# Kernel optimization log

Measured on AMD Instinct MI355X. Metric: run time of the kernel, lower is better.

## Reference

```python
import jax, jax.numpy as jnp
import numpy as np

N = 100000      # total nodes (flattened batch)
E = 640000      # total edges
D = 128         # in_channels
SIM_THR = 0.2   # pt_dict['sim_pt']
DEG_THR = 3.0   # pt_dict['degree_pt']
PT_THRESHOLD = 0.1  # edge-pruning cosine threshold
EPS = 1e-8      # F.cosine_similarity eps


def _glorot(key, shape):
    a = np.sqrt(6.0 / (shape[-2] + shape[-1]))
    return jax.random.uniform(key, shape, jnp.float32, -a, a)


def setup_inputs() -> dict:
    key = jax.random.key(0)
    k1, k2, k3, k4, k5 = jax.random.split(key, 5)
    x = jax.random.normal(k1, (N, D), jnp.float32)
    edge_index = jax.random.randint(k2, (2, E), 0, N, dtype=jnp.int32)
    p_sim = _glorot(k3, (1, D))
    p_deg = _glorot(k4, (1, D))
    p_other = _glorot(k5, (1, D))
    return {"x": x, "edge_index": edge_index, "p_sim": p_sim, "p_deg": p_deg, "p_other": p_other}


def reference(x, edge_index, p_sim, p_deg, p_other):
    n = x.shape[0]
    row, col = edge_index[0], edge_index[1]

    # --- sim_pt: per-edge cosine of raw features, scatter-add to dst, degree-normalize ---
    x_norm = x / jnp.sqrt(jnp.sum(x * x, axis=1, keepdims=True))          # [N, D]
    e = jnp.sum(x_norm[row] * x_norm[col], axis=1)                         # [E]
    c = jax.ops.segment_sum(e, col, num_segments=n)                        # [N]
    deg = jax.ops.segment_sum(jnp.ones_like(e), col, num_segments=n)       # [N]
    # torch: c/deg -> nan for deg==0, nan <= thr is False; +inf gives the same mask, safely.
    csim = jnp.where(deg > 0, c / jnp.maximum(deg, 1.0), jnp.inf)
    mask_sim = csim <= SIM_THR                                             # [N]

    # --- degree_pt ---
    mask_deg = deg <= DEG_THR                                              # [N]

    # --- other_pt == 'all': nodes that got no prompt so far ---
    mask_other = ~(mask_sim | mask_deg)                                    # [N]

    # g_mutiftpt_record: [N, 3, D], slot filled with its prompt row where mask else 0
    masks = jnp.stack([mask_sim, mask_deg, mask_other], axis=1)            # [N, 3]
    prompts = jnp.concatenate([p_sim, p_deg, p_other], axis=0)             # [3, D]
    record = masks[:, :, None].astype(x.dtype) * prompts[None, :, :]       # [N, 3, D]

    # use_attention=False branch: mean over non-padding (all-nonzero) slots
    wo_pad = jnp.all(record != 0, axis=-1)                                 # [N, 3]
    plen = jnp.sum(wo_pad, axis=1, keepdims=True).astype(x.dtype)          # [N, 1]
    final = jnp.where(plen > 0, record.sum(axis=1) / jnp.maximum(plen, 1.0), 0.0)  # [N, D]

    x_new = x + final                                                      # add_pt

    # edge pruning by cosine similarity of prompted features (F.cosine_similarity, eps=1e-8)
    nrm = jnp.sqrt(jnp.sum(x_new * x_new, axis=1))                         # [N]
    na = jnp.maximum(nrm[row], EPS)
    nb = jnp.maximum(nrm[col], EPS)
    cos = jnp.sum(x_new[row] * x_new[col], axis=1) / (na * nb)             # [E]
    keep_edges = cos >= PT_THRESHOLD                                       # [E] bool mask (edge list is static-shape; mask instead of compaction)
    return x_new, keep_edges
```

## Files before the change

### kernel.cpp

```cpp
#include <hip/hip_runtime.h>
#include <hip/hip_bf16.h>
#include <math.h>

#define D_DIM 128
#define SIM_THR 0.2f
#define DEG_THR 3.0f
#define PT_THR 0.1
#define EPS_CS 1e-8
#define MARGIN 4e-3f
#define PK 4294967296.0

typedef unsigned short u16;

#define WS_NEED 8960064

__device__ __forceinline__ float bf2f(u16 u) {
    return __uint_as_float(((unsigned)u) << 16);
}

__global__ void prompt_pre_kernel(const float* __restrict__ ps,
                                  const float* __restrict__ pd,
                                  const float* __restrict__ po,
                                  int* __restrict__ flags,
                                  float* __restrict__ G) {
    int t = threadIdx.x;
    float s0 = ps[t], s1 = ps[t + 64];
    float d0 = pd[t], d1 = pd[t + 64];
    float o0 = po[t], o1 = po[t + 64];
    float ss = s0 * s0 + s1 * s1;
    float sd = s0 * d0 + s1 * d1;
    float so = s0 * o0 + s1 * o1;
    float dd = d0 * d0 + d1 * d1;
    float dO = d0 * o0 + d1 * o1;
    float oo = o0 * o0 + o1 * o1;
    for (int m = 32; m; m >>= 1) {
        ss += __shfl_xor(ss, m);
        sd += __shfl_xor(sd, m);
        so += __shfl_xor(so, m);
        dd += __shfl_xor(dd, m);
        dO += __shfl_xor(dO, m);
        oo += __shfl_xor(oo, m);
    }
    unsigned long long zs = __ballot(s0 == 0.0f || s1 == 0.0f);
    unsigned long long zd = __ballot(d0 == 0.0f || d1 == 0.0f);
    unsigned long long zo = __ballot(o0 == 0.0f || o1 == 0.0f);
    if (t == 0) {
        flags[0] = (zs == 0ull);
        flags[1] = (zd == 0ull);
        flags[2] = (zo == 0ull);
        G[0] = ss; G[1] = sd; G[2] = so;
        G[3] = sd; G[4] = dd; G[5] = dO;
        G[6] = so; G[7] = dO; G[8] = oo;
    }
}

__global__ void node_pre_kernel(const float* __restrict__ x,
                                const float* __restrict__ ps,
                                const float* __restrict__ pd,
                                const float* __restrict__ po,
                                u16* __restrict__ xnorm,
                                float* __restrict__ nx,
                                float* __restrict__ rs,
                                float* __restrict__ rd,
                                float* __restrict__ ro, int N) {
    int g = threadIdx.x >> 5;
    int lane = threadIdx.x & 31;
    int n = blockIdx.x * 8 + g;
    if (n >= N) return;
    int off = lane * 4;
    const float4 v = *(const float4*)(x + (size_t)n * D_DIM + off);
    const float4 s = *(const float4*)(ps + off);
    const float4 d = *(const float4*)(pd + off);
    const float4 o = *(const float4*)(po + off);
    float sq = v.x * v.x + v.y * v.y + v.z * v.z + v.w * v.w;
    float drs = v.x * s.x + v.y * s.y + v.z * s.z + v.w * s.w;
    float drd = v.x * d.x + v.y * d.y + v.z * d.z + v.w * d.w;
    float dro = v.x * o.x + v.y * o.y + v.z * o.z + v.w * o.w;
    for (int m = 16; m; m >>= 1) {
        sq += __shfl_xor(sq, m, 32);
        drs += __shfl_xor(drs, m, 32);
        drd += __shfl_xor(drd, m, 32);
        dro += __shfl_xor(dro, m, 32);
    }
    float nrm = sqrtf(sq);
    float inv = 1.0f / nrm;
    __hip_bfloat16 ob[4];
    ob[0] = __float2bfloat16(v.x * inv);
    ob[1] = __float2bfloat16(v.y * inv);
    ob[2] = __float2bfloat16(v.z * inv);
    ob[3] = __float2bfloat16(v.w * inv);
    *(ushort4*)(xnorm + (size_t)n * D_DIM + off) =
        make_ushort4(*(u16*)&ob[0], *(u16*)&ob[1], *(u16*)&ob[2], *(u16*)&ob[3]);
    if (lane == 0) {
        nx[n] = nrm;
        rs[n] = drs;
        rd[n] = drd;
        ro[n] = dro;
    }
}

__global__ void edge_sim_kernel(const u16* __restrict__ xnorm,
                                const int* __restrict__ ei,
                                double* __restrict__ cd,
                                float* __restrict__ e_arr,
                                int E) {
    int lane = threadIdx.x & 31;
    int grp = blockIdx.x * 8 + (threadIdx.x >> 5);
    int base = grp * 4;
    if (base >= E) return;

    int r[4], c4[4];
    #pragma unroll
    for (int k = 0; k < 4; ++k) {
        int e = base + k;
        int src = (e < E) ? e : base;
        r[k] = ei[src];
        c4[k] = ei[E + src];
    }

    ushort4 a[4], b[4];
    #pragma unroll
    for (int k = 0; k < 4; ++k) {
        a[k] = *(const ushort4*)(xnorm + (size_t)r[k] * D_DIM + lane * 4);
        b[k] = *(const ushort4*)(xnorm + (size_t)c4[k] * D_DIM + lane * 4);
    }

    float d[4];
    #pragma unroll
    for (int k = 0; k < 4; ++k) {
        d[k] = bf2f(a[k].x) * bf2f(b[k].x) + bf2f(a[k].y) * bf2f(b[k].y) +
               bf2f(a[k].z) * bf2f(b[k].z) + bf2f(a[k].w) * bf2f(b[k].w);
    }
    for (int m = 16; m; m >>= 1) {
        #pragma unroll
        for (int k = 0; k < 4; ++k) d[k] += __shfl_xor(d[k], m, 32);
    }

    if (lane < 4) {
        int e = base + lane;
        if (e < E) {
            float dv = (lane == 0) ? d[0] : (lane == 1) ? d[1] : (lane == 2) ? d[2] : d[3];
            if (e_arr) e_arr[e] = dv;
            atomicAdd(&cd[c4[lane]], (double)dv + PK);
        }
    }
}

__global__ void node_prompt_kernel(const float* __restrict__ x,
                                   const double* __restrict__ cd,
                                   const float* __restrict__ ps,
                                   const float* __restrict__ pd,
                                   const float* __restrict__ po,
                                   const int* __restrict__ flags,
                                   const float* __restrict__ nx,
                                   const float* __restrict__ rs,
                                   const float* __restrict__ rd,
                                   const float* __restrict__ ro,
                                   float* __restrict__ xn,
                                   double* __restrict__ na,
                                   float* __restrict__ pack, int N) {
    int g = threadIdx.x >> 5;
    int lane = threadIdx.x & 31;
    int n = blockIdx.x * 8 + g;
    if (n >= N) return;
    double v = cd[n];
    double degd = floor(v * (1.0 / PK) + 0.5);
    float dg = (float)degd;
    float cc = (float)(v - degd * PK);
    float csim = (dg > 0.0f) ? (cc / fmaxf(dg, 1.0f)) : INFINITY;
    bool ms = (csim <= SIM_THR);
    bool md = (dg <= DEG_THR);
    bool mo = !(ms || md);
    int plen = (ms && flags[0]) + (md && flags[1]) + (mo && flags[2]);
    float invp = (plen > 0) ? (1.0f / (float)plen) : 0.0f;

    int off = lane * 4;
    const float4 xv = *(const float4*)(x + (size_t)n * D_DIM + off);
    const float4 s  = *(const float4*)(ps + off);
    const float4 dd = *(const float4*)(pd + off);
    const float4 o  = *(const float4*)(po + off);

    float4 f;
    f.x = (ms ? s.x : 0.0f) + (md ? dd.x : 0.0f) + (mo ? o.x : 0.0f);
    f.y = (ms ? s.y : 0.0f) + (md ? dd.y : 0.0f) + (mo ? o.y : 0.0f);
    f.z = (ms ? s.z : 0.0f) + (md ? dd.z : 0.0f) + (mo ? o.z : 0.0f);
    f.w = (ms ? s.w : 0.0f) + (md ? dd.w : 0.0f) + (mo ? o.w : 0.0f);

    float4 r;
    r.x = xv.x + f.x * invp;
    r.y = xv.y + f.y * invp;
    r.z = xv.z + f.z * invp;
    r.w = xv.w + f.w * invp;

    *(float4*)(xn + (size_t)n * D_DIM + off) = r;

    double sq = (double)r.x * r.x + (double)r.y * r.y + (double)r.z * r.z + (double)r.w * r.w;
    for (int m = 16; m; m >>= 1) sq += __shfl_xor(sq, m, 32);
    if (lane == 0) {
        double nrm = sqrt(sq);
        double nad = (nrm > EPS_CS) ? nrm : EPS_CS;
        na[n] = nad;
        if (pack) {
            float as = ms ? invp : 0.0f;
            float ad = md ? invp : 0.0f;
            float ao = mo ? invp : 0.0f;
            float4 w0 = make_float4(rs[n], rd[n], ro[n], nx[n]);
            float4 w1 = make_float4(as, ad, ao, (float)(1.0 / nad));
            *(float4*)(pack + (size_t)n * 8)     = w0;
            *(float4*)(pack + (size_t)n * 8 + 4) = w1;
        }
    }
}

__global__ void edge_prune_fused(const int* __restrict__ ei,
                                 const float* __restrict__ e_arr,
                                 const float* __restrict__ pack,
                                 const float* __restrict__ G,
                                 const float* __restrict__ xn,
                                 const double* __restrict__ na,
                                 float* __restrict__ keep, int E) {
    __shared__ int s_list[256];
    __shared__ int s_cnt;
    int tid = threadIdx.x;
    if (tid == 0) s_cnt = 0;
    __syncthreads();

    int e = blockIdx.x * 256 + tid;
    if (e < E) {
        int i = ei[e], j = ei[E + e];
        const float4 ri = *(const float4*)(pack + (size_t)i * 8);
        const float4 ai = *(const float4*)(pack + (size_t)i * 8 + 4);
        const float4 rj = *(const float4*)(pack + (size_t)j * 8);
        const float4 aj = *(const float4*)(pack + (size_t)j * 8 + 4);
        float ev = e_arr[e];
        float dot = ev * ri.w * rj.w
                  + aj.x * ri.x + aj.y * ri.y + aj.z * ri.z
                  + ai.x * rj.x + ai.y * rj.y + ai.z * rj.z;
        dot += ai.x * (G[0] * aj.x + G[1] * aj.y + G[2] * aj.z)
             + ai.y * (G[3] * aj.x + G[4] * aj.y + G[5] * aj.z)
             + ai.z * (G[6] * aj.x + G[7] * aj.y + G[8] * aj.z);
        float cosv = dot * ai.w * aj.w;
        keep[e] = (cosv >= 0.1f) ? 1.0f : 0.0f;
        if (fabsf(cosv - 0.1f) < MARGIN) {
            int idx = atomicAdd(&s_cnt, 1);
            s_list[idx] = e;
        }
    }
    __syncthreads();

    int cnt = s_cnt;
    int lane = tid & 31;
    int grp = tid >> 5;
    for (int it = grp; it < cnt; it += 8) {
        int ee = s_list[it];
        int row = ei[ee], col = ei[E + ee];
        const float4 a = *(const float4*)(xn + (size_t)row * D_DIM + lane * 4);
        const float4 b = *(const float4*)(xn + (size_t)col * D_DIM + lane * 4);
        double d = (double)a.x * b.x + (double)a.y * b.y +
                   (double)a.z * b.z + (double)a.w * b.w;
        for (int m = 16; m; m >>= 1) d += __shfl_xor(d, m, 32);
        if (lane == 0) {
            double cs = d / (na[row] * na[col]);
            keep[ee] = (cs >= PT_THR) ? 1.0f : 0.0f;
        }
    }
}

__global__ void edge_prune_kernel(const float* __restrict__ xn,
                                  const int* __restrict__ ei,
                                  const double* __restrict__ na,
                                  float* __restrict__ keep, int E) {
    int lane = threadIdx.x & 31;
    int grp = blockIdx.x * 8 + (threadIdx.x >> 5);
    int e0 = grp * 2, e1 = e0 + 1;
    if (e0 >= E) return;
    bool has1 = (e1 < E);
    int row0 = ei[e0], col0 = ei[E + e0];
    int row1 = has1 ? ei[e1] : row0;
    int col1 = has1 ? ei[E + e1] : col0;

    const float4 a0 = *(const float4*)(xn + (size_t)row0 * D_DIM + lane * 4);
    const float4 b0 = *(const float4*)(xn + (size_t)col0 * D_DIM + lane * 4);
    const float4 a1 = *(const float4*)(xn + (size_t)row1 * D_DIM + lane * 4);
    const float4 b1 = *(const float4*)(xn + (size_t)col1 * D_DIM + lane * 4);

    double d0 = (double)a0.x * b0.x + (double)a0.y * b0.y +
                (double)a0.z * b0.z + (double)a0.w * b0.w;
    double d1 = (double)a1.x * b1.x + (double)a1.y * b1.y +
                (double)a1.z * b1.z + (double)a1.w * b1.w;
    for (int m = 16; m; m >>= 1) {
        d0 += __shfl_xor(d0, m, 32);
        d1 += __shfl_xor(d1, m, 32);
    }
    if (lane == 0) {
        double cs = d0 / (na[row0] * na[col0]);
        keep[e0] = (cs >= PT_THR) ? 1.0f : 0.0f;
    } else if (lane == 1 && has1) {
        double cs = d1 / (na[row1] * na[col1]);
        keep[e1] = (cs >= PT_THR) ? 1.0f : 0.0f;
    }
}

extern "C" void kernel_launch(void* const* d_in, const int* in_sizes, int n_in,
                              void* d_out, int out_size, void* d_ws, size_t ws_size,
                              hipStream_t stream) {
    const float* x  = (const float*)d_in[0];
    const int*   ei = (const int*)d_in[1];
    const float* ps = (const float*)d_in[2];
    const float* pd = (const float*)d_in[3];
    const float* po = (const float*)d_in[4];

    const int N = in_sizes[0] / D_DIM;
    const int E = in_sizes[1] / 2;

    float* xn    = (float*)d_out;
    float* keep  = (float*)d_out + (size_t)N * D_DIM;
    u16*   xnorm = (u16*)d_out;

    char* ws = (char*)d_ws;
    const int nodeBlocks = (N + 7) / 8;
    const int simBlocks  = (E + 31) / 32;

    if (ws_size >= (size_t)WS_NEED) {
        double* cd    = (double*)(ws + 0);
        double* na    = (double*)(ws + 800000);
        float* nx     = (float*)(ws + 1600000);
        float* rs     = (float*)(ws + 2000000);
        float* rd     = (float*)(ws + 2400000);
        float* ro     = (float*)(ws + 2800000);
        float* e_arr  = (float*)(ws + 3200000);
        float* pack   = (float*)(ws + 5760000);
        int*   flags  = (int*)(ws + 8960000);
        float* G      = (float*)(ws + 8960016);

        hipMemsetAsync(cd, 0, 800000, stream);

        prompt_pre_kernel<<<1, 64, 0, stream>>>(ps, pd, po, flags, G);
        node_pre_kernel<<<nodeBlocks, 256, 0, stream>>>(x, ps, pd, po, xnorm, nx, rs, rd, ro, N);
        edge_sim_kernel<<<simBlocks, 256, 0, stream>>>(xnorm, ei, cd, e_arr, E);
        node_prompt_kernel<<<nodeBlocks, 256, 0, stream>>>(x, cd, ps, pd, po,
                                                           flags, nx, rs, rd, ro,
                                                           xn, na, pack, N);
        edge_prune_fused<<<(E + 255) / 256, 256, 0, stream>>>(ei, e_arr, pack, G, xn, na, keep, E);
    } else {
        double* cd    = (double*)(ws + 0);
        double* na    = (double*)(ws + 800000);
        int*   flags  = (int*)(ws + 1600000);
        float* G      = (float*)(ws + 1600016);
        float* scratch = (float*)(ws + 1600064);

        hipMemsetAsync(cd, 0, 800000, stream);
        prompt_pre_kernel<<<1, 64, 0, stream>>>(ps, pd, po, flags, G);
        node_pre_kernel<<<nodeBlocks, 256, 0, stream>>>(x, ps, pd, po, xnorm,
                                                        scratch, scratch, scratch, scratch, N);
        edge_sim_kernel<<<simBlocks, 256, 0, stream>>>(xnorm, ei, cd, nullptr, E);
        node_prompt_kernel<<<nodeBlocks, 256, 0, stream>>>(x, cd, ps, pd, po,
                                                           flags, nullptr, nullptr, nullptr, nullptr,
                                                           xn, na, nullptr, N);
        edge_prune_kernel<<<(E + 15) / 16, 256, 0, stream>>>(xn, ei, na, keep, E);
    }
}
```

Before: 107.6 us.

## Quantize normalized features to fp8 with exact fixup for near-threshold nodes

Normalized node features are stored as packed fp8 e4m3 instead of bf16, which halves the gather traffic in the edge similarity pass. Per-edge similarities are saved as bf16. Nodes whose mean similarity falls within a margin of the threshold are marked in a bitmap, then recomputed exactly by a scan over all edges and a node fixup kernel. The memset and the prompt-precompute launch are folded into the first node kernel, and the prune-candidate list is bounded with an inline exact fallback when it overflows. In exchange this adds two extra launches, including a full edge scan, and relies on a fixed margin being wide enough to cover the fp8 error.

Result: slower. 115.6 us (+7.4%).

```diff
diff --git a/kernel.cpp b/kernel.cpp
--- a/kernel.cpp
+++ b/kernel.cpp
@@ -1,5 +1,6 @@
 #include <hip/hip_runtime.h>
 #include <hip/hip_bf16.h>
+#include <hip/hip_fp8.h>
 #include <math.h>
 
 #define D_DIM 128
@@ -7,103 +8,114 @@
 #define DEG_THR 3.0f
 #define PT_THR 0.1
 #define EPS_CS 1e-8
-#define MARGIN 4e-3f
+#define NODE_MARGIN 0.022f
+#define PRUNE_MARGIN 0.022f
 #define PK 4294967296.0
 
 typedef unsigned short u16;
-
-#define WS_NEED 8960064
+typedef unsigned int u32;
+
+#define WS_NEED 8092900
 
 __device__ __forceinline__ float bf2f(u16 u) {
-    return __uint_as_float(((unsigned)u) << 16);
-}
-
-__global__ void prompt_pre_kernel(const float* __restrict__ ps,
-                                  const float* __restrict__ pd,
-                                  const float* __restrict__ po,
-                                  int* __restrict__ flags,
-                                  float* __restrict__ G) {
-    int t = threadIdx.x;
-    float s0 = ps[t], s1 = ps[t + 64];
-    float d0 = pd[t], d1 = pd[t + 64];
-    float o0 = po[t], o1 = po[t + 64];
-    float ss = s0 * s0 + s1 * s1;
-    float sd = s0 * d0 + s1 * d1;
-    float so = s0 * o0 + s1 * o1;
-    float dd = d0 * d0 + d1 * d1;
-    float dO = d0 * o0 + d1 * o1;
-    float oo = o0 * o0 + o1 * o1;
-    for (int m = 32; m; m >>= 1) {
-        ss += __shfl_xor(ss, m);
-        sd += __shfl_xor(sd, m);
-        so += __shfl_xor(so, m);
-        dd += __shfl_xor(dd, m);
-        dO += __shfl_xor(dO, m);
-        oo += __shfl_xor(oo, m);
-    }
-    unsigned long long zs = __ballot(s0 == 0.0f || s1 == 0.0f);
-    unsigned long long zd = __ballot(d0 == 0.0f || d1 == 0.0f);
-    unsigned long long zo = __ballot(o0 == 0.0f || o1 == 0.0f);
-    if (t == 0) {
-        flags[0] = (zs == 0ull);
-        flags[1] = (zd == 0ull);
-        flags[2] = (zo == 0ull);
-        G[0] = ss; G[1] = sd; G[2] = so;
-        G[3] = sd; G[4] = dd; G[5] = dO;
-        G[6] = so; G[7] = dO; G[8] = oo;
-    }
-}
-
-__global__ void node_pre_kernel(const float* __restrict__ x,
-                                const float* __restrict__ ps,
-                                const float* __restrict__ pd,
-                                const float* __restrict__ po,
-                                u16* __restrict__ xnorm,
-                                float* __restrict__ nx,
-                                float* __restrict__ rs,
-                                float* __restrict__ rd,
-                                float* __restrict__ ro, int N) {
+    return __uint_as_float(((u32)u) << 16);
+}
+__device__ __forceinline__ float f8f(u32 v) {
+    __hip_fp8_e4m3 t;
+    t.__x = (__hip_fp8_storage_t)v;
+    return (float)t;
+}
+__device__ __forceinline__ u16 f2bf(float f) {
+    __hip_bfloat16 b = __float2bfloat16(f);
+    return *(u16*)&b;
+}
+
+__global__ void node_pre_fp8(const float* __restrict__ x,
+                             const float* __restrict__ ps,
+                             const float* __restrict__ pd,
+                             const float* __restrict__ po,
+                             u32* __restrict__ x8d,
+                             float* __restrict__ nx,
+                             float* __restrict__ rs,
+                             float* __restrict__ rd,
+                             float* __restrict__ ro,
+                             double* __restrict__ cd,
+                             u32* __restrict__ bitmap, int nbmw,
+                             int* __restrict__ flags,
+                             float* __restrict__ G, int N) {
     int g = threadIdx.x >> 5;
     int lane = threadIdx.x & 31;
     int n = blockIdx.x * 8 + g;
-    if (n >= N) return;
-    int off = lane * 4;
-    const float4 v = *(const float4*)(x + (size_t)n * D_DIM + off);
-    const float4 s = *(const float4*)(ps + off);
-    const float4 d = *(const float4*)(pd + off);
-    const float4 o = *(const float4*)(po + off);
-    float sq = v.x * v.x + v.y * v.y + v.z * v.z + v.w * v.w;
-    float drs = v.x * s.x + v.y * s.y + v.z * s.z + v.w * s.w;
-    float drd = v.x * d.x + v.y * d.y + v.z * d.z + v.w * d.w;
-    float dro = v.x * o.x + v.y * o.y + v.z * o.z + v.w * o.w;
-    for (int m = 16; m; m >>= 1) {
-        sq += __shfl_xor(sq, m, 32);
-        drs += __shfl_xor(drs, m, 32);
-        drd += __shfl_xor(drd, m, 32);
-        dro += __shfl_xor(dro, m, 32);
-    }
-    float nrm = sqrtf(sq);
-    float inv = 1.0f / nrm;
-    __hip_bfloat16 ob[4];
-    ob[0] = __float2bfloat16(v.x * inv);
-    ob[1] = __float2bfloat16(v.y * inv);
-    ob[2] = __float2bfloat16(v.z * inv);
-    ob[3] = __float2bfloat16(v.w * inv);
-    *(ushort4*)(xnorm + (size_t)n * D_DIM + off) =
-        make_ushort4(*(u16*)&ob[0], *(u16*)&ob[1], *(u16*)&ob[2], *(u16*)&ob[3]);
-    if (lane == 0) {
-        nx[n] = nrm;
-        rs[n] = drs;
-        rd[n] = drd;
-        ro[n] = dro;
-    }
-}
-
-__global__ void edge_sim_kernel(const u16* __restrict__ xnorm,
-                                const int* __restrict__ ei,
-                                double* __restrict__ cd,
-                                float* __restrict__ e_arr,
-                                int E) {
+    int gid = blockIdx.x * 256 + threadIdx.x;
+    if (gid < nbmw) bitmap[gid] = 0u;
+    if (n < N) {
+        int off = lane * 4;
+        const float4 v = *(const float4*)(x + (size_t)n * D_DIM + off);
+        const float4 s = *(const float4*)(ps + off);
+        const float4 d = *(const float4*)(pd + off);
+        const float4 o = *(const float4*)(po + off);
+        float sq = v.x * v.x + v.y * v.y + v.z * v.z + v.w * v.w;
+        float drs = v.x * s.x + v.y * s.y + v.z * s.z + v.w * s.w;
+        float drd = v.x * d.x + v.y * d.y + v.z * d.z + v.w * d.w;
+        float dro = v.x * o.x + v.y * o.y + v.z * o.z + v.w * o.w;
+        for (int m = 16; m; m >>= 1) {
+            sq += __shfl_xor(sq, m, 32);
+            drs += __shfl_xor(drs, m, 32);
+            drd += __shfl_xor(drd, m, 32);
+            dro += __shfl_xor(dro, m, 32);
+        }
+        float nrm = sqrtf(sq);
+        float inv = 1.0f / nrm;
+        __hip_fp8_e4m3 q0(v.x * inv), q1(v.y * inv), q2(v.z * inv), q3(v.w * inv);
+        u32 packed = (u32)q0.__x | ((u32)q1.__x << 8) |
+                     ((u32)q2.__x << 16) | ((u32)q3.__x << 24);
+        x8d[(size_t)n * 32 + lane] = packed;
+        if (lane == 0) {
+            nx[n] = nrm;
+            rs[n] = drs;
+            rd[n] = drd;
+            ro[n] = dro;
+            cd[n] = 0.0;
+        }
+    }
+    if (blockIdx.x == 0 && threadIdx.x < 64) {
+        int t = threadIdx.x;
+        float s0 = ps[t], s1 = ps[t + 64];
+        float d0 = pd[t], d1 = pd[t + 64];
+        float o0 = po[t], o1 = po[t + 64];
+        float ss = s0 * s0 + s1 * s1;
+        float sd = s0 * d0 + s1 * d1;
+        float so = s0 * o0 + s1 * o1;
+        float dd = d0 * d0 + d1 * d1;
+        float dO = d0 * o0 + d1 * o1;
+        float oo = o0 * o0 + o1 * o1;
+        for (int m = 32; m; m >>= 1) {
+            ss += __shfl_xor(ss, m);
+            sd += __shfl_xor(sd, m);
+            so += __shfl_xor(so, m);
+            dd += __shfl_xor(dd, m);
+            dO += __shfl_xor(dO, m);
+            oo += __shfl_xor(oo, m);
+        }
+        unsigned long long zs = __ballot(s0 == 0.0f || s1 == 0.0f);
+        unsigned long long zd = __ballot(d0 == 0.0f || d1 == 0.0f);
+        unsigned long long zo = __ballot(o0 == 0.0f || o1 == 0.0f);
+        if (t == 0) {
+            flags[0] = (zs == 0ull);
+            flags[1] = (zd == 0ull);
+            flags[2] = (zo == 0ull);
+            G[0] = ss; G[1] = sd; G[2] = so;
+            G[3] = sd; G[4] = dd; G[5] = dO;
+            G[6] = so; G[7] = dO; G[8] = oo;
+        }
+    }
+}
+
+__global__ void edge_sim_fp8(const u32* __restrict__ x8d,
+                             const int* __restrict__ ei,
+                             double* __restrict__ cd,
+                             u16* __restrict__ e_arr,
+                             int E) {
     int lane = threadIdx.x & 31;
     int grp = blockIdx.x * 8 + (threadIdx.x >> 5);
     int base = grp * 4;
@@ -117,30 +129,30 @@
         r[k] = ei[src];
         c4[k] = ei[E + src];
     }
-
-    ushort4 a[4], b[4];
+    u32 a[4], b[4];
     #pragma unroll
     for (int k = 0; k < 4; ++k) {
-        a[k] = *(const ushort4*)(xnorm + (size_t)r[k] * D_DIM + lane * 4);
-        b[k] = *(const ushort4*)(xnorm + (size_t)c4[k] * D_DIM + lane * 4);
-    }
-
+        a[k] = x8d[(size_t)r[k] * 32 + lane];
+        b[k] = x8d[(size_t)c4[k] * 32 + lane];
+    }
     float d[4];
     #pragma unroll
     for (int k = 0; k < 4; ++k) {
-        d[k] = bf2f(a[k].x) * bf2f(b[k].x) + bf2f(a[k].y) * bf2f(b[k].y) +
-               bf2f(a[k].z) * bf2f(b[k].z) + bf2f(a[k].w) * bf2f(b[k].w);
+        d[k] = f8f(a[k] & 255u) * f8f(b[k] & 255u) +
+               f8f((a[k] >> 8) & 255u) * f8f((b[k] >> 8) & 255u) +
+               f8f((a[k] >> 16) & 255u) * f8f((b[k] >> 16) & 255u) +
+               f8f(a[k] >> 24) * f8f(b[k] >> 24);
     }
     for (int m = 16; m; m >>= 1) {
         #pragma unroll
         for (int k = 0; k < 4; ++k) d[k] += __shfl_xor(d[k], m, 32);
     }
-
     if (lane < 4) {
         int e = base + lane;
         if (e < E) {
-            float dv = (lane == 0) ? d[0] : (lane == 1) ? d[1] : (lane == 2) ? d[2] : d[3];
-            if (e_arr) e_arr[e] = dv;
+            float dv = (lane == 0) ? d[0] : (lane == 1) ? d[1]
+                     : (lane == 2) ? d[2] : d[3];
+            e_arr[e] = f2bf(dv);
             atomicAdd(&cd[c4[lane]], (double)dv + PK);
         }
     }
@@ -158,7 +170,9 @@
                                    const float* __restrict__ ro,
                                    float* __restrict__ xn,
                                    double* __restrict__ na,
-                                   float* __restrict__ pack, int N) {
+                                   float* __restrict__ pack,
+                                   u32* __restrict__ bitmap,
+                                   float* __restrict__ cfix, int N) {
     int g = threadIdx.x >> 5;
     int lane = threadIdx.x & 31;
     int n = blockIdx.x * 8 + g;
@@ -200,20 +214,107 @@
         double nrm = sqrt(sq);
         double nad = (nrm > EPS_CS) ? nrm : EPS_CS;
         na[n] = nad;
-        if (pack) {
-            float as = ms ? invp : 0.0f;
-            float ad = md ? invp : 0.0f;
-            float ao = mo ? invp : 0.0f;
-            float4 w0 = make_float4(rs[n], rd[n], ro[n], nx[n]);
-            float4 w1 = make_float4(as, ad, ao, (float)(1.0 / nad));
-            *(float4*)(pack + (size_t)n * 8)     = w0;
-            *(float4*)(pack + (size_t)n * 8 + 4) = w1;
-        }
+        float as = ms ? invp : 0.0f;
+        float ad = md ? invp : 0.0f;
+        float ao = mo ? invp : 0.0f;
+        *(float4*)(pack + (size_t)n * 8)     = make_float4(rs[n], rd[n], ro[n], nx[n]);
+        *(float4*)(pack + (size_t)n * 8 + 4) = make_float4(as, ad, ao, (float)(1.0 / nad));
+        if (dg > 0.0f && fabsf(csim - SIM_THR) < NODE_MARGIN) {
+            cfix[n] = 0.0f;
+            atomicOr(&bitmap[n >> 5], 1u << (n & 31));
+        }
+    }
+}
+
+__global__ void edge_fix_scan(const float* __restrict__ x,
+                              const int* __restrict__ ei,
+                              const float* __restrict__ nx,
+                              const u32* __restrict__ bitmap,
+                              float* __restrict__ cfix, int E) {
+    int e = blockIdx.x * 256 + threadIdx.x;
+    if (e >= E) return;
+    int col = ei[E + e];
+    if (!((bitmap[col >> 5] >> (col & 31)) & 1u)) return;
+    int row = ei[e];
+    const float4* xr = (const float4*)(x + (size_t)row * D_DIM);
+    const float4* xc = (const float4*)(x + (size_t)col * D_DIM);
+    double s = 0.0;
+    for (int i = 0; i < 32; ++i) {
+        float4 a = xr[i], b = xc[i];
+        s += (double)a.x * b.x + (double)a.y * b.y +
+             (double)a.z * b.z + (double)a.w * b.w;
+    }
+    float ev = (float)(s / ((double)nx[row] * (double)nx[col]));
+    atomicAdd(&cfix[col], ev);
+}
+
+__global__ void node_fix_kernel(const float* __restrict__ x,
+                                const double* __restrict__ cd,
+                                const float* __restrict__ cfix,
+                                const u32* __restrict__ bitmap,
+                                const float* __restrict__ ps,
+                                const float* __restrict__ pd,
+                                const float* __restrict__ po,
+                                const int* __restrict__ flags,
+                                const float* __restrict__ nx,
+                                const float* __restrict__ rs,
+                                const float* __restrict__ rd,
+                                const float* __restrict__ ro,
+                                float* __restrict__ xn,
+                                double* __restrict__ na,
+                                float* __restrict__ pack, int N) {
+    int g = threadIdx.x >> 5;
+    int lane = threadIdx.x & 31;
+    int n = blockIdx.x * 8 + g;
+    if (n >= N) return;
+    if (!((bitmap[n >> 5] >> (n & 31)) & 1u)) return;
+
+    double v = cd[n];
+    double degd = floor(v * (1.0 / PK) + 0.5);
+    float dg = (float)degd;
+    float csim = cfix[n] / fmaxf(dg, 1.0f);
+    bool ms = (csim <= SIM_THR);
+    bool md = (dg <= DEG_THR);
+    bool mo = !(ms || md);
+    int plen = (ms && flags[0]) + (md && flags[1]) + (mo && flags[2]);
+    float invp = (plen > 0) ? (1.0f / (float)plen) : 0.0f;
+
+    int off = lane * 4;
+    const float4 xv = *(const float4*)(x + (size_t)n * D_DIM + off);
+    const float4 s  = *(const float4*)(ps + off);
+    const float4 dd = *(const float4*)(pd + off);
+    const float4 o  = *(const float4*)(po + off);
+
+    float4 f;
+    f.x = (ms ? s.x : 0.0f) + (md ? dd.x : 0.0f) + (mo ? o.x : 0.0f);
+    f.y = (ms ? s.y : 0.0f) + (md ? dd.y : 0.0f) + (mo ? o.y : 0.0f);
+    f.z = (ms ? s.z : 0.0f) + (md ? dd.z : 0.0f) + (mo ? o.z : 0.0f);
+    f.w = (ms ? s.w : 0.0f) + (md ? dd.w : 0.0f) + (mo ? o.w : 0.0f);
+
+    float4 r;
+    r.x = xv.x + f.x * invp;
+    r.y = xv.y + f.y * invp;
+    r.z = xv.z + f.z * invp;
+    r.w = xv.w + f.w * invp;
+
+    *(float4*)(xn + (size_t)n * D_DIM + off) = r;
+
+    double sq = (double)r.x * r.x + (double)r.y * r.y + (double)r.z * r.z + (double)r.w * r.w;
+    for (int m = 16; m; m >>= 1) sq += __shfl_xor(sq, m, 32);
+    if (lane == 0) {
+        double nrm = sqrt(sq);
+        double nad = (nrm > EPS_CS) ? nrm : EPS_CS;
+        na[n] = nad;
+        float as = ms ? invp : 0.0f;
+        float ad = md ? invp : 0.0f;
+        float ao = mo ? invp : 0.0f;
+        *(float4*)(pack + (size_t)n * 8)     = make_float4(rs[n], rd[n], ro[n], nx[n]);
+        *(float4*)(pack + (size_t)n * 8 + 4) = make_float4(as, ad, ao, (float)(1.0 / nad));
     }
 }
 
 __global__ void edge_prune_fused(const int* __restrict__ ei,
-                                 const float* __restrict__ e_arr,
+                                 const u16* __restrict__ e_arr,
                                  const float* __restrict__ pack,
                                  const float* __restrict__ G,
                                  const float* __restrict__ xn,
@@ -232,7 +333,7 @@
         const float4 ai = *(const float4*)(pack + (size_t)i * 8 + 4);
         const float4 rj = *(const float4*)(pack + (size_t)j * 8);
         const float4 aj = *(const float4*)(pack + (size_t)j * 8 + 4);
-        float ev = e_arr[e];
+        float ev = bf2f(e_arr[e]);
         float dot = ev * ri.w * rj.w
                   + aj.x * ri.x + aj.y * ri.y + aj.z * ri.z
                   + ai.x * rj.x + ai.y * rj.y + ai.z * rj.z;
@@ -241,14 +342,27 @@
              + ai.z * (G[6] * aj.x + G[7] * aj.y + G[8] * aj.z);
         float cosv = dot * ai.w * aj.w;
         keep[e] = (cosv >= 0.1f) ? 1.0f : 0.0f;
-        if (fabsf(cosv - 0.1f) < MARGIN) {
+        if (fabsf(cosv - 0.1f) < PRUNE_MARGIN) {
             int idx = atomicAdd(&s_cnt, 1);
-            s_list[idx] = e;
+            if (idx < 256) {
+                s_list[idx] = e;
+            } else {
+                const float4* xr = (const float4*)(xn + (size_t)i * D_DIM);
+                const float4* xc = (const float4*)(xn + (size_t)j * D_DIM);
+                double sd = 0.0;
+                for (int it = 0; it < 32; ++it) {
+                    float4 a = xr[it], b = xc[it];
+                    sd += (double)a.x * b.x + (double)a.y * b.y +
+                          (double)a.z * b.z + (double)a.w * b.w;
+                }
+                double cs = sd / (na[i] * na[j]);
+                keep[e] = (cs >= PT_THR) ? 1.0f : 0.0f;
+            }
         }
     }
     __syncthreads();
 
-    int cnt = s_cnt;
+    int cnt = s_cnt < 256 ? s_cnt : 256;
     int lane = tid & 31;
     int grp = tid >> 5;
     for (int it = grp; it < cnt; it += 8) {
@@ -266,10 +380,121 @@
     }
 }
 
-__global__ void edge_prune_kernel(const float* __restrict__ xn,
-                                  const int* __restrict__ ei,
-                                  const double* __restrict__ na,
-                                  float* __restrict__ keep, int E) {
+__global__ void node_pre_bf16(const float* __restrict__ x,
+                              const float* __restrict__ ps,
+                              const float* __restrict__ pd,
+                              const float* __restrict__ po,
+                              u16* __restrict__ xnorm,
+                              double* __restrict__ cd,
+                              int* __restrict__ flags, int N) {
+    int g = threadIdx.x >> 5;
+    int lane = threadIdx.x & 31;
+    int n = blockIdx.x * 8 + g;
+    if (n < N) {
+        int off = lane * 4;
+        const float4 v = *(const float4*)(x + (size_t)n * D_DIM + off);
+        float sq = v.x * v.x + v.y * v.y + v.z * v.z + v.w * v.w;
+        for (int m = 16; m; m >>= 1) sq += __shfl_xor(sq, m, 32);
+        float inv = 1.0f / sqrtf(sq);
+        *(ushort4*)(xnorm + (size_t)n * D_DIM + off) =
+            make_ushort4(f2bf(v.x * inv), f2bf(v.y * inv), f2bf(v.z * inv), f2bf(v.w * inv));
+        if (lane == 0) cd[n] = 0.0;
+    }
+    if (blockIdx.x == 0 && threadIdx.x < 64) {
+        int t = threadIdx.x;
+        unsigned long long zs = __ballot(ps[t] == 0.0f || ps[t + 64] == 0.0f);
+        unsigned long long zd = __ballot(pd[t] == 0.0f || pd[t + 64] == 0.0f);
+        unsigned long long zo = __ballot(po[t] == 0.0f || po[t + 64] == 0.0f);
+        if (t == 0) {
+            flags[0] = (zs == 0ull);
+            flags[1] = (zd == 0ull);
+            flags[2] = (zo == 0ull);
+        }
+    }
+}
+
+__global__ void edge_sim_bf16(const u16* __restrict__ xnorm,
+                              const int* __restrict__ ei,
+                              double* __restrict__ cd, int E) {
+    int lane = threadIdx.x & 31;
+    int grp = blockIdx.x * 8 + (threadIdx.x >> 5);
+    int base = grp * 4;
+    if (base >= E) return;
+    int r[4], c4[4];
+    #pragma unroll
+    for (int k = 0; k < 4; ++k) {
+        int e = base + k;
+        int src = (e < E) ? e : base;
+        r[k] = ei[src];
+        c4[k] = ei[E + src];
+    }
+    float d[4];
+    #pragma unroll
+    for (int k = 0; k < 4; ++k) {
+        ushort4 a = *(const ushort4*)(xnorm + (size_t)r[k] * D_DIM + lane * 4);
+        ushort4 b = *(const ushort4*)(xnorm + (size_t)c4[k] * D_DIM + lane * 4);
+        d[k] = bf2f(a.x) * bf2f(b.x) + bf2f(a.y) * bf2f(b.y) +
+               bf2f(a.z) * bf2f(b.z) + bf2f(a.w) * bf2f(b.w);
+    }
+    for (int m = 16; m; m >>= 1) {
+        #pragma unroll
+        for (int k = 0; k < 4; ++k) d[k] += __shfl_xor(d[k], m, 32);
+    }
+    if (lane < 4) {
+        int e = base + lane;
+        if (e < E) {
+            float dv = (lane == 0) ? d[0] : (lane == 1) ? d[1]
+                     : (lane == 2) ? d[2] : d[3];
+            atomicAdd(&cd[c4[lane]], (double)dv + PK);
+        }
+    }
+}
+
+__global__ void node_prompt_fb(const float* __restrict__ x,
+                               const double* __restrict__ cd,
+                               const float* __restrict__ ps,
+                               const float* __restrict__ pd,
+                               const float* __restrict__ po,
+                               const int* __restrict__ flags,
+                               float* __restrict__ xn,
+                               double* __restrict__ na, int N) {
+    int g = threadIdx.x >> 5;
+    int lane = threadIdx.x & 31;
+    int n = blockIdx.x * 8 + g;
+    if (n >= N) return;
+    double v = cd[n];
+    double degd = floor(v * (1.0 / PK) + 0.5);
+    float dg = (float)degd;
+    float cc = (float)(v - degd * PK);
+    float csim = (dg > 0.0f) ? (cc / fmaxf(dg, 1.0f)) : INFINITY;
+    bool ms = (csim <= SIM_THR);
+    bool md = (dg <= DEG_THR);
+    bool mo = !(ms || md);
+    int plen = (ms && flags[0]) + (md && flags[1]) + (mo && flags[2]);
+    float invp = (plen > 0) ? (1.0f / (float)plen) : 0.0f;
+    int off = lane * 4;
+    const float4 xv = *(const float4*)(x + (size_t)n * D_DIM + off);
+    const float4 s  = *(const float4*)(ps + off);
+    const float4 dd = *(const float4*)(pd + off);
+    const float4 o  = *(const float4*)(po + off);
+    float4 r;
+    r.x = xv.x + ((ms ? s.x : 0.0f) + (md ? dd.x : 0.0f) + (mo ? o.x : 0.0f)) * invp;
+    r.y = xv.y + ((ms ? s.y : 0.0f) + (md ? dd.y : 0.0f) + (mo ? o.y : 0.0f)) * invp;
+    r.z = xv.z + ((ms ? s.z : 0.0f) + (md ? dd.z : 0.0f) + (mo ? o.z : 0.0f)) * invp;
+    r.w = xv.w + ((ms ? s.w : 0.0f) + (md ? dd.w : 0.0f) + (mo ? o.w : 0.0f)) * invp;
+    *(float4*)(xn + (size_t)n * D_DIM + off) = r;
+    double sq = (double)r.x * r.x + (double)r.y * r.y + (double)r.z * r.z + (double)r.w * r.w;
+    for (int m = 16; m; m >>= 1) sq += __shfl_xor(sq, m, 32);
+    if (lane == 0) {
+        double nrm = sqrt(sq);
+        na[n] = (nrm > EPS_CS) ? nrm : EPS_CS;
+    }
+}
+
+__global__ void edge_prune_exact(const float* __restrict__ xn,
+                                 const int* __restrict__ ei,
+                                 const double* __restrict__ na,
+                                 float* __restrict__ keep, int E) {
     int lane = threadIdx.x & 31;
     int grp = blockIdx.x * 8 + (threadIdx.x >> 5);
     int e0 = grp * 2, e1 = e0 + 1;
@@ -278,12 +503,10 @@
     int row0 = ei[e0], col0 = ei[E + e0];
     int row1 = has1 ? ei[e1] : row0;
     int col1 = has1 ? ei[E + e1] : col0;
-
     const float4 a0 = *(const float4*)(xn + (size_t)row0 * D_DIM + lane * 4);
     const float4 b0 = *(const float4*)(xn + (size_t)col0 * D_DIM + lane * 4);
     const float4 a1 = *(const float4*)(xn + (size_t)row1 * D_DIM + lane * 4);
     const float4 b1 = *(const float4*)(xn + (size_t)col1 * D_DIM + lane * 4);
-
     double d0 = (double)a0.x * b0.x + (double)a0.y * b0.y +
                 (double)a0.z * b0.z + (double)a0.w * b0.w;
     double d1 = (double)a1.x * b1.x + (double)a1.y * b1.y +
@@ -293,11 +516,9 @@
         d1 += __shfl_xor(d1, m, 32);
     }
     if (lane == 0) {
-        double cs = d0 / (na[row0] * na[col0]);
-        keep[e0] = (cs >= PT_THR) ? 1.0f : 0.0f;
+        keep[e0] = ((d0 / (na[row0] * na[col0])) >= PT_THR) ? 1.0f : 0.0f;
     } else if (lane == 1 && has1) {
-        double cs = d1 / (na[row1] * na[col1]);
-        keep[e1] = (cs >= PT_THR) ? 1.0f : 0.0f;
+        keep[e1] = ((d1 / (na[row1] * na[col1])) >= PT_THR) ? 1.0f : 0.0f;
     }
 }
 
@@ -313,13 +534,12 @@
     const int N = in_sizes[0] / D_DIM;
     const int E = in_sizes[1] / 2;
 
-    float* xn    = (float*)d_out;
-    float* keep  = (float*)d_out + (size_t)N * D_DIM;
-    u16*   xnorm = (u16*)d_out;
+    float* xn   = (float*)d_out;
+    float* keep = (float*)d_out + (size_t)N * D_DIM;
 
     char* ws = (char*)d_ws;
     const int nodeBlocks = (N + 7) / 8;
-    const int simBlocks  = (E + 31) / 32;
+    const int nbmw = (N + 31) / 32;
 
     if (ws_size >= (size_t)WS_NEED) {
         double* cd    = (double*)(ws + 0);
@@ -328,35 +548,35 @@
         float* rs     = (float*)(ws + 2000000);
         float* rd     = (float*)(ws + 2400000);
         float* ro     = (float*)(ws + 2800000);
-        float* e_arr  = (float*)(ws + 3200000);
-        float* pack   = (float*)(ws + 5760000);
-        int*   flags  = (int*)(ws + 8960000);
-        float* G      = (float*)(ws + 8960016);
-
-        hipMemsetAsync(cd, 0, 800000, stream);
-
-        prompt_pre_kernel<<<1, 64, 0, stream>>>(ps, pd, po, flags, G);
-        node_pre_kernel<<<nodeBlocks, 256, 0, stream>>>(x, ps, pd, po, xnorm, nx, rs, rd, ro, N);
-        edge_sim_kernel<<<simBlocks, 256, 0, stream>>>(xnorm, ei, cd, e_arr, E);
-        node_prompt_kernel<<<nodeBlocks, 256, 0, stream>>>(x, cd, ps, pd, po,
-                                                           flags, nx, rs, rd, ro,
-                                                           xn, na, pack, N);
-        edge_prune_fused<<<(E + 255) / 256, 256, 0, stream>>>(ei, e_arr, pack, G, xn, na, keep, E);
+        u16*   e_arr  = (u16*)(ws + 3200000);
+        float* pack   = (float*)(ws + 4480000);
+        float* cfix   = (float*)(ws + 7680000);
+        u32*   bitmap = (u32*)(ws + 8080000);
+        int*   flags  = (int*)(ws + 8092800);
+        float* G      = (float*)(ws + 8092816);
+        u32*   x8d    = (u32*)d_out;
+
+        node_pre_fp8<<<nodeBlocks, 256, 0, stream>>>(x, ps, pd, po, x8d, nx, rs, rd, ro,
+                                                     cd, bitmap, nbmw, flags, G, N);
+        edge_sim_fp8<<<(E + 31) / 32, 256, 0, stream>>>(x8d, ei, cd, e_arr, E);
+        node_prompt_kernel<<<nodeBlocks, 256, 0, stream>>>(x, cd, ps, pd, po, flags,
+                                                           nx, rs, rd, ro,
+                                                           xn, na, pack, bitmap, cfix, N);
+        edge_fix_scan<<<(E + 255) / 256, 256, 0, stream>>>(x, ei, nx, bitmap, cfix, E);
+        node_fix_kernel<<<nodeBlocks, 256, 0, stream>>>(x, cd, cfix, bitmap, ps, pd, po,
+                                                        flags, nx, rs, rd, ro,
+                                                        xn, na, pack, N);
+        edge_prune_fused<<<(E + 255) / 256, 256, 0, stream>>>(ei, e_arr, pack, G,
+                                                              xn, na, keep, E);
     } else {
         double* cd    = (double*)(ws + 0);
         double* na    = (double*)(ws + 800000);
-        int*   flags  = (int*)(ws + 1600000);
-        float* G      = (float*)(ws + 1600016);
-        float* scratch = (float*)(ws + 1600064);
-
-        hipMemsetAsync(cd, 0, 800000, stream);
-        prompt_pre_kernel<<<1, 64, 0, stream>>>(ps, pd, po, flags, G);
-        node_pre_kernel<<<nodeBlocks, 256, 0, stream>>>(x, ps, pd, po, xnorm,
-                                                        scratch, scratch, scratch, scratch, N);
-        edge_sim_kernel<<<simBlocks, 256, 0, stream>>>(xnorm, ei, cd, nullptr, E);
-        node_prompt_kernel<<<nodeBlocks, 256, 0, stream>>>(x, cd, ps, pd, po,
-                                                           flags, nullptr, nullptr, nullptr, nullptr,
-                                                           xn, na, nullptr, N);
-        edge_prune_kernel<<<(E + 15) / 16, 256, 0, stream>>>(xn, ei, na, keep, E);
-    }
-}
+        int*    flags = (int*)(ws + 1600000);
+        u16*    xnorm = (u16*)d_out;
+
+        node_pre_bf16<<<nodeBlocks, 256, 0, stream>>>(x, ps, pd, po, xnorm, cd, flags, N);
+        edge_sim_bf16<<<(E + 31) / 32, 256, 0, stream>>>(xnorm, ei, cd, E);
+        node_prompt_fb<<<nodeBlocks, 256, 0, stream>>>(x, cd, ps, pd, po, flags, xn, na, N);
+        edge_prune_exact<<<(E + 15) / 16, 256, 0, stream>>>(xn, ei, na, keep, E);
+    }
+}
```
